# Kernel tuning notes

Measured on AMD Instinct MI355X. Metric: run time of the kernel, lower is better.

## Reference

```python
import jax, jax.numpy as jnp
import numpy as np

D_MODEL = 256
N_LEVELS = 4
N_HEADS = 8
N_POINTS = 4
HEAD_DIM = D_MODEL // N_HEADS
SPATIAL_SHAPES = np.array([[128, 128], [64, 64], [32, 32], [16, 16]], dtype=np.int64)
LEN_IN = int((SPATIAL_SHAPES[:, 0] * SPATIAL_SHAPES[:, 1]).sum())  # 21760
BATCH = 2
LEN_Q = LEN_IN  # encoder self-attention


def setup_inputs() -> dict:
    key = jax.random.key(0)
    ks = jax.random.split(key, 12)
    C = D_MODEL
    lvl_start = np.concatenate([[0], np.cumsum(SPATIAL_SHAPES[:, 0] * SPATIAL_SHAPES[:, 1])[:-1]]).astype(np.int64)
    return {
        'query': jax.random.normal(ks[0], (BATCH, LEN_Q, C), jnp.float32),
        'reference_points': jax.random.uniform(ks[1], (BATCH, LEN_Q, N_LEVELS, 2), jnp.float32),
        'input_flatten': jax.random.normal(ks[2], (BATCH, LEN_IN, C), jnp.float32),
        'input_spatial_shapes': SPATIAL_SHAPES,          # static numpy: shapes must be concrete
        'input_level_start_index': lvl_start,            # static numpy
        'Wv': jax.random.normal(ks[3], (C, C), jnp.float32) / np.sqrt(C),
        'bv': jnp.zeros((C,), jnp.float32),
        'Woff': jax.random.normal(ks[4], (C, N_HEADS * N_LEVELS * N_POINTS * 2), jnp.float32) * 0.01,
        'boff': jax.random.normal(ks[5], (N_HEADS * N_LEVELS * N_POINTS * 2,), jnp.float32) * 0.5,
        'Wa': jax.random.normal(ks[6], (C, N_HEADS * N_LEVELS * N_POINTS), jnp.float32) * 0.01,
        'ba': jnp.zeros((N_HEADS * N_LEVELS * N_POINTS,), jnp.float32),
        'Wo': jax.random.normal(ks[7], (C, C), jnp.float32) / np.sqrt(C),
        'bo': jnp.zeros((C,), jnp.float32),
    }


def _grid_sample_bilinear(v, grid):
    """v: (B,H,W,D); grid: (B,Q,P,2) in [-1,1] (x,y). align_corners=False, zero padding."""
    B, H, W, D = v.shape
    x = (grid[..., 0] + 1.0) * 0.5 * W - 0.5
    y = (grid[..., 1] + 1.0) * 0.5 * H - 0.5
    x0 = jnp.floor(x)
    y0 = jnp.floor(y)
    wx = x - x0
    wy = y - y0
    b = jnp.arange(B)[:, None, None]

    def corner(xi, yi, w):
        valid = (xi >= 0) & (xi < W) & (yi >= 0) & (yi < H)
        xi_ = jnp.clip(xi, 0, W - 1).astype(jnp.int32)
        yi_ = jnp.clip(yi, 0, H - 1).astype(jnp.int32)
        return v[b, yi_, xi_] * (w * valid)[..., None]  # (B,Q,P,D)

    return (corner(x0, y0, (1 - wx) * (1 - wy))
            + corner(x0 + 1, y0, wx * (1 - wy))
            + corner(x0, y0 + 1, (1 - wx) * wy)
            + corner(x0 + 1, y0 + 1, wx * wy))


def _msdeform_attn(query, reference_points, input_flatten, spatial_shapes_np,
                   Wv, bv, Woff, boff, Wa, ba, Wo, bo):
    N, Lq, C = query.shape
    Lin = input_flatten.shape[1]
    M, L, P, D = N_HEADS, N_LEVELS, N_POINTS, HEAD_DIM

    value = (input_flatten @ Wv + bv).reshape(N, Lin, M, D)
    offsets = (query @ Woff + boff).reshape(N, Lq, M, L, P, 2)
    attn = jax.nn.softmax((query @ Wa + ba).reshape(N, Lq, M, L * P), axis=-1).reshape(N, Lq, M, L, P)

    # sampling locations in [0,1] -> grid in [-1,1]
    grids = 2.0 * (reference_points[:, :, None, :, None, :] + offsets) - 1.0  # (N,Lq,M,L,P,2)

    out = jnp.zeros((N * M, Lq, D), value.dtype)
    start = 0
    for lid in range(L):
        H_, W_ = int(spatial_shapes_np[lid, 0]), int(spatial_shapes_np[lid, 1])
        v_l = value[:, start:start + H_ * W_]                       # (N,HW,M,D)
        v_l = v_l.transpose(0, 2, 1, 3).reshape(N * M, H_, W_, D)   # (N*M,H,W,D)
        g_l = grids[:, :, :, lid].transpose(0, 2, 1, 3, 4).reshape(N * M, Lq, P, 2)
        sampled = _grid_sample_bilinear(v_l, g_l)                   # (N*M,Lq,P,D)
        a_l = attn[:, :, :, lid].transpose(0, 2, 1, 3).reshape(N * M, Lq, P)
        out = out + jnp.einsum('bqpd,bqp->bqd', sampled, a_l)
        start += H_ * W_

    out = out.reshape(N, M, Lq, D).transpose(0, 2, 1, 3).reshape(N, Lq, M * D)
    return out @ Wo + bo


def reference(query, reference_points, input_flatten, input_spatial_shapes,
              input_level_start_index, Wv, bv, Woff, boff, Wa, ba, Wo, bo):
    spatial_np = np.asarray(input_spatial_shapes)
    return _msdeform_attn(query, reference_points, input_flatten, spatial_np,
                          Wv, bv, Woff, boff, Wa, ba, Wo, bo)
```

## Files before the change

### kernel.cpp

```cpp
#include <hip/hip_runtime.h>
#include <cstdint>
#include <cstddef>

#define LEN_IN  21760
#define BATCH   2
#define MROWS   (BATCH * LEN_IN)

typedef _Float16 hv8 __attribute__((ext_vector_type(8)));
typedef float    fv4 __attribute__((ext_vector_type(4)));

#define WAIT_LGKM0() __builtin_amdgcn_s_waitcnt(0xC07F)
#define RAW_BARRIER() __builtin_amdgcn_s_barrier()

__global__ __launch_bounds__(256) void cvt_weights(
    const float* __restrict__ Wv, const float* __restrict__ Woff,
    const float* __restrict__ Wa, const float* __restrict__ Wo,
    _Float16* __restrict__ WvT, _Float16* __restrict__ WoffT2,
    _Float16* __restrict__ WaT, _Float16* __restrict__ WoT)
{
  __shared__ float t[64][65];
  const int id = blockIdx.x, tid = threadIdx.x;
  const int c = tid & 63, r4 = tid >> 6;

  const float* src; _Float16* dst; int N; bool split = false; int nt, kt;
  if (id < 16)      { src = Wv;   dst = WvT;    N = 256; nt = id & 3;        kt = id >> 2; }
  else if (id < 32) { src = Woff; dst = WoffT2; N = 256; nt = (id - 16) & 3; kt = (id - 16) >> 2; split = true; }
  else if (id < 40) { src = Wa;   dst = WaT;    N = 128; nt = (id - 32) & 1; kt = (id - 32) >> 1; }
  else              { src = Wo;   dst = WoT;    N = 256; nt = (id - 40) & 3; kt = (id - 40) >> 2; }
  const int nb = nt * 64, kb = kt * 64;

#pragma unroll
  for (int rr = 0; rr < 16; ++rr) {
    const int r = rr * 4 + r4;
    t[r][c] = src[(size_t)(kb + r) * N + nb + c];
  }
  __syncthreads();
#pragma unroll
  for (int rr = 0; rr < 16; ++rr) {
    const int r = rr * 4 + r4;
    const float v = t[c][r];
    const _Float16 h = (_Float16)v;
    dst[(size_t)(nb + r) * 256 + kb + c] = h;
    if (split)
      dst[(size_t)(256 + nb + r) * 256 + kb + c] = (_Float16)(v - (float)h);
  }
}

template<int NTOT, int AF32, int OUTMODE>
__global__ __launch_bounds__(256) void gemm_pipe(
    const void* __restrict__ Ap, const _Float16* __restrict__ Bt,
    const float* __restrict__ bias, void* __restrict__ Cout)
{
  __shared__ _Float16 As[2][64 * 40];
  __shared__ _Float16 Bs[2][128 * 40];

  const int tid = threadIdx.x, lane = tid & 63, wave = tid >> 6;
  const int l15 = lane & 15, quad = lane >> 4;
  const int wc = wave * 32;
  const int rowBase = blockIdx.x * 64;
  const int colBase = blockIdx.y * 128;
  const int rs = tid >> 2, ks = (tid & 3) * 8;

  const float*    A32 = (const float*)Ap;
  const _Float16* A16 = (const _Float16*)Ap;

  float4 pa[3][2]; hv8 pa16[3]; hv8 pb[2][2];

  auto issueA = [&](int it) {
    const int k0 = it * 32, s = it % 3;
    if constexpr (AF32) {
      pa[s][0] = *(const float4*)&A32[(size_t)(rowBase + rs) * 256 + k0 + ks];
      pa[s][1] = *(const float4*)&A32[(size_t)(rowBase + rs) * 256 + k0 + ks + 4];
    } else {
      pa16[s] = *(const hv8*)&A16[(size_t)(rowBase + rs) * 256 + k0 + ks];
    }
  };
  auto issueB = [&](int it) {
    const int k0 = it * 32, s = it & 1;
#pragma unroll
    for (int p = 0; p < 2; ++p)
      pb[s][p] = *(const hv8*)&Bt[(size_t)(colBase + p * 64 + rs) * 256 + k0 + ks];
  };

  issueA(0); issueB(0); issueA(1); issueB(1); issueA(2);

  fv4 acc[4][2] = {};

#pragma unroll
  for (int it = 0; it < 8; ++it) {
    const int sb = it & 1, sa = it % 3;
    if constexpr (AF32) {
      const float4 f0 = pa[sa][0], f1 = pa[sa][1];
      const float fa[8] = {f0.x, f0.y, f0.z, f0.w, f1.x, f1.y, f1.z, f1.w};
      hv8 h;
#pragma unroll
      for (int e = 0; e < 8; ++e) h[e] = (_Float16)fa[e];
      *(hv8*)&As[sb][rs * 40 + ks] = h;
    } else {
      *(hv8*)&As[sb][rs * 40 + ks] = pa16[sa];
    }
#pragma unroll
    for (int p = 0; p < 2; ++p)
      *(hv8*)&Bs[sb][(p * 64 + rs) * 40 + ks] = pb[sb][p];
    if (it + 2 < 8) issueB(it + 2);
    if (it + 3 < 8) issueA(it + 3);
    WAIT_LGKM0();
    RAW_BARRIER();

    hv8 af[4];
#pragma unroll
    for (int i = 0; i < 4; ++i)
      af[i] = *(const hv8*)&As[sb][(i * 16 + l15) * 40 + quad * 8];
#pragma unroll
    for (int j = 0; j < 2; ++j) {
      const hv8 bf = *(const hv8*)&Bs[sb][(wc + j * 16 + l15) * 40 + quad * 8];
#pragma unroll
      for (int i = 0; i < 4; ++i)
        acc[i][j] = __builtin_amdgcn_mfma_f32_16x16x32_f16(af[i], bf, acc[i][j], 0, 0, 0);
    }
  }

#pragma unroll
  for (int j = 0; j < 2; ++j) {
    const int col = colBase + wc + j * 16 + l15;
    const float bj = bias[col];
#pragma unroll
    for (int i = 0; i < 4; ++i)
#pragma unroll
      for (int rg = 0; rg < 4; ++rg) {
        const int row = rowBase + i * 16 + quad * 4 + rg;
        const float v = acc[i][j][rg] + bj;
        if constexpr (OUTMODE == 0) {
          ((float*)Cout)[(size_t)row * NTOT + col] = v;
        } else if constexpr (OUTMODE == 1) {
          ((_Float16*)Cout)[(size_t)row * NTOT + col] = (_Float16)v;
        } else {
          const int n = (row >= LEN_IN) ? 1 : 0;
          const int pix = row - n * LEN_IN;
          const int m = col >> 5, d = col & 31;
          ((_Float16*)Cout)[((size_t)(n * 8 + m) * LEN_IN + pix) * 32 + d] = (_Float16)v;
        }
      }
  }
}

__global__ __launch_bounds__(256) void gemm_offs_pipe(
    const float* __restrict__ A, const _Float16* __restrict__ B2,
    const float* __restrict__ boff, const float* __restrict__ refpts,
    float* __restrict__ C)
{
  __shared__ _Float16 Ash[64 * 40], Asl[64 * 40];
  __shared__ _Float16 Bs[256 * 40];

  const int tid = threadIdx.x, lane = tid & 63, wave = tid >> 6;
  const int l15 = lane & 15, quad = lane >> 4;
  const int wc = wave * 32;
  const int rowBase = blockIdx.x * 64;
  const int colBase = blockIdx.y * 128;
  const int rs = tid >> 2, ks = (tid & 3) * 8;

  float4 pa[3][2]; hv8 pb[2][4];

  auto issueA = [&](int it) {
    const int k0 = it * 32, s = it % 3;
    pa[s][0] = *(const float4*)&A[(size_t)(rowBase + rs) * 256 + k0 + ks];
    pa[s][1] = *(const float4*)&A[(size_t)(rowBase + rs) * 256 + k0 + ks + 4];
  };
  auto issueB = [&](int it) {
    const int k0 = it * 32, s = it & 1;
#pragma unroll
    for (int p = 0; p < 4; ++p) {
      const int grow = (p < 2) ? (colBase + p * 64 + rs)
                               : (256 + colBase + (p - 2) * 64 + rs);
      pb[s][p] = *(const hv8*)&B2[(size_t)grow * 256 + k0 + ks];
    }
  };

  issueA(0); issueB(0); issueA(1); issueB(1); issueA(2);

  fv4 acc[4][2] = {};

#pragma unroll
  for (int it = 0; it < 8; ++it) {
    const int sa = it % 3, s2 = it & 1;
    {
      const float4 f0 = pa[sa][0], f1 = pa[sa][1];
      const float fa[8] = {f0.x, f0.y, f0.z, f0.w, f1.x, f1.y, f1.z, f1.w};
      hv8 hh, ll;
#pragma unroll
      for (int e = 0; e < 8; ++e) {
        hh[e] = (_Float16)fa[e];
        ll[e] = (_Float16)(fa[e] - (float)hh[e]);
      }
      *(hv8*)&Ash[rs * 40 + ks] = hh;
      *(hv8*)&Asl[rs * 40 + ks] = ll;
    }
#pragma unroll
    for (int p = 0; p < 4; ++p)
      *(hv8*)&Bs[(p * 64 + rs) * 40 + ks] = pb[s2][p];
    if (it + 2 < 8) issueB(it + 2);
    if (it + 3 < 8) issueA(it + 3);
    WAIT_LGKM0();
    RAW_BARRIER();

    hv8 ah[4], al[4];
#pragma unroll
    for (int i = 0; i < 4; ++i) {
      ah[i] = *(const hv8*)&Ash[(i * 16 + l15) * 40 + quad * 8];
      al[i] = *(const hv8*)&Asl[(i * 16 + l15) * 40 + quad * 8];
    }
#pragma unroll
    for (int j = 0; j < 2; ++j) {
      const hv8 bh = *(const hv8*)&Bs[(wc + j * 16 + l15) * 40 + quad * 8];
      const hv8 bl = *(const hv8*)&Bs[(128 + wc + j * 16 + l15) * 40 + quad * 8];
#pragma unroll
      for (int i = 0; i < 4; ++i) {
        acc[i][j] = __builtin_amdgcn_mfma_f32_16x16x32_f16(ah[i], bh, acc[i][j], 0, 0, 0);
        acc[i][j] = __builtin_amdgcn_mfma_f32_16x16x32_f16(ah[i], bl, acc[i][j], 0, 0, 0);
        acc[i][j] = __builtin_amdgcn_mfma_f32_16x16x32_f16(al[i], bh, acc[i][j], 0, 0, 0);
      }
    }
    WAIT_LGKM0();
    RAW_BARRIER();
  }

#pragma unroll
  for (int j = 0; j < 2; ++j) {
    const int c = colBase + wc + j * 16 + l15;
    const int xy = c & 1, l = (c >> 3) & 3;
    const float Wl = (float)(128 >> l);
    const float bj = boff[c];
#pragma unroll
    for (int i = 0; i < 4; ++i)
#pragma unroll
      for (int rg = 0; rg < 4; ++rg) {
        const int row = rowBase + i * 16 + quad * 4 + rg;
        const float ref = refpts[(size_t)row * 8 + l * 2 + xy];
        C[(size_t)row * 256 + c] = (acc[i][j][rg] + bj + ref) * Wl - 0.5f;
      }
  }
}

__global__ __launch_bounds__(256, 6) void sample_kernel(
    const _Float16* __restrict__ value16,
    const float* __restrict__ coords,
    const _Float16* __restrict__ logits16,
    _Float16* __restrict__ outp16)
{
  __shared__ unsigned s_pair[4096];
  __shared__ float    s_attn[1024];

  const int tid = threadIdx.x;
  const int qBase = blockIdx.x * 8;

  if (tid < 64) {
    const hv8* lp = (const hv8*)&logits16[(size_t)(qBase + (tid >> 3)) * 128 + (tid & 7) * 16];
    const hv8 w0 = lp[0], w1 = lp[1];
    float w[16];
#pragma unroll
    for (int e = 0; e < 8; ++e) { w[e] = (float)w0[e]; w[8 + e] = (float)w1[e]; }
    float mx = w[0];
#pragma unroll
    for (int i = 1; i < 16; ++i) mx = fmaxf(mx, w[i]);
    float sum = 0.f;
#pragma unroll
    for (int i = 0; i < 16; ++i) { w[i] = expf(w[i] - mx); sum += w[i]; }
    const float inv = 1.f / sum;
#pragma unroll
    for (int p = 0; p < 16; ++p) s_attn[p * 64 + tid] = w[p] * inv;
  }
  __syncthreads();

#pragma unroll
  for (int k = 0; k < 4; ++k) {
    const int i = tid + 256 * k;
    const int p = i >> 6, q = (i >> 3) & 7, m = i & 7;
    const int l = p >> 2, pp = p & 3;
    const int qg = qBase + q;
    const float2 of = *(const float2*)&coords[(size_t)qg * 256 + ((m * 4 + l) * 4 + pp) * 2];
    const float aw = s_attn[i];
    const int W = 128 >> l;
    const int st = (l == 0) ? 0 : (l == 1) ? 16384 : (l == 2) ? 20480 : 21504;
    const float xf = floorf(of.x), yf = floorf(of.y);
    const int x0 = (int)xf, y0 = (int)yf;
    const float wx = of.x - xf, wy = of.y - yf;
    uint4 rec;
    unsigned* rp = &rec.x;
#pragma unroll
    for (int c = 0; c < 4; ++c) {
      const int dx = c & 1, dy = c >> 1;
      const int xi = x0 + dx, yi = y0 + dy;
      const bool valid = (xi >= 0) & (xi < W) & (yi >= 0) & (yi < W);
      const float w = (dx ? wx : 1.f - wx) * (dy ? wy : 1.f - wy) * aw;
      union { _Float16 h; unsigned short s; } pk;
      pk.h = (_Float16)w;
      const unsigned idx = (unsigned)(st + yi * W + xi);
      rp[c] = valid ? (idx | ((unsigned)pk.s << 16)) : 0u;
    }
    *(uint4*)&s_pair[i * 4] = rec;
  }
  __syncthreads();

  const int wave = tid >> 6, lane = tid & 63;
  const int qloc = wave * 2 + (lane >> 5);
  const int sub = lane & 31, m = sub >> 2, j = sub & 3;
  const int qg = qBase + qloc;
  const int n = (qg >= LEN_IN) ? 1 : 0;
  const char* base = (const char*)value16 + (size_t)(n * 8 + m) * LEN_IN * 64 + j * 16;
  const int lb = qloc * 8 + m;

  float acc8[8] = {0.f, 0.f, 0.f, 0.f, 0.f, 0.f, 0.f, 0.f};
#pragma unroll 4
  for (int p = 0; p < 16; ++p) {
    const uint4 u4 = *(const uint4*)&s_pair[(p * 64 + lb) * 4];
    const unsigned uu[4] = {u4.x, u4.y, u4.z, u4.w};
#pragma unroll
    for (int c = 0; c < 4; ++c) {
      const unsigned u = uu[c];
      union { unsigned short s; _Float16 h; } pk;
      pk.s = (unsigned short)(u >> 16);
      const float w = (float)pk.h;
      const hv8 v = *(const hv8*)(base + (size_t)(u & 32767u) * 64);
#pragma unroll
      for (int e = 0; e < 8; ++e) acc8[e] = fmaf(w, (float)v[e], acc8[e]);
    }
  }

  hv8 o;
#pragma unroll
  for (int e = 0; e < 8; ++e) o[e] = (_Float16)acc8[e];
  *(hv8*)&outp16[(size_t)qg * 256 + m * 32 + j * 8] = o;
}

extern "C" void kernel_launch(void* const* d_in, const int* in_sizes, int n_in,
                              void* d_out, int out_size, void* d_ws, size_t ws_size,
                              hipStream_t stream) {
  const float* query   = (const float*)d_in[0];
  const float* refpts  = (const float*)d_in[1];
  const float* flatten = (const float*)d_in[2];
  const float* Wv   = (const float*)d_in[5];
  const float* bv   = (const float*)d_in[6];
  const float* Woff = (const float*)d_in[7];
  const float* boff = (const float*)d_in[8];
  const float* Wa   = (const float*)d_in[9];
  const float* ba   = (const float*)d_in[10];
  const float* Wo   = (const float*)d_in[11];
  const float* bo   = (const float*)d_in[12];
  float* out = (float*)d_out;

  const size_t NE = (size_t)MROWS * 256;
  _Float16* value16  = (_Float16*)d_ws;
  float*    coords   = (float*)(value16 + NE);
  _Float16* logits16 = (_Float16*)(coords + NE);
  _Float16* outp16   = logits16 + NE / 2;
  _Float16* WvT      = outp16 + NE;
  _Float16* WoffT2   = WvT + 256 * 256;
  _Float16* WaT      = WoffT2 + 512 * 256;
  _Float16* WoT      = WaT + 128 * 256;

  const dim3 blk(256);
  const int mtiles = MROWS / 64;

  cvt_weights<<<dim3(56), blk, 0, stream>>>(Wv, Woff, Wa, Wo, WvT, WoffT2, WaT, WoT);

  gemm_pipe<256, 1, 2><<<dim3(mtiles, 2), blk, 0, stream>>>(flatten, WvT, bv, value16);
  gemm_offs_pipe<<<dim3(mtiles, 2), blk, 0, stream>>>(query, WoffT2, boff, refpts, coords);
  gemm_pipe<128, 1, 1><<<dim3(mtiles, 1), blk, 0, stream>>>(query, WaT, ba, logits16);
  sample_kernel<<<dim3(MROWS / 8), blk, 0, stream>>>(value16, coords, logits16, outp16);
  gemm_pipe<256, 0, 0><<<dim3(mtiles, 2), blk, 0, stream>>>(outp16, WoT, bo, out);
}
```

Before: 283.8 us.

## Pre-convert activations to fp16 and fuse input GEMMs using direct global-to-LDS loads

```diff
diff --git a/kernel.cpp b/kernel.cpp
--- a/kernel.cpp
+++ b/kernel.cpp
@@ -9,8 +9,16 @@
 typedef _Float16 hv8 __attribute__((ext_vector_type(8)));
 typedef float    fv4 __attribute__((ext_vector_type(4)));
 
+#define AS1 __attribute__((address_space(1)))
+#define AS3 __attribute__((address_space(3)))
+
+#define WAIT_VM(N)   __builtin_amdgcn_s_waitcnt(0x0F70 | (N))
 #define WAIT_LGKM0() __builtin_amdgcn_s_waitcnt(0xC07F)
-#define RAW_BARRIER() __builtin_amdgcn_s_barrier()
+#define BAR()        __builtin_amdgcn_s_barrier()
+
+__device__ __forceinline__ void gl_lds16(const _Float16* g, _Float16* l) {
+  __builtin_amdgcn_global_load_lds((const AS1 void*)g, (AS3 void*)l, 16, 0, 0);
+}
 
 __global__ __launch_bounds__(256) void cvt_weights(
     const float* __restrict__ Wv, const float* __restrict__ Woff,
@@ -46,187 +54,148 @@
   }
 }
 
-template<int NTOT, int AF32, int OUTMODE>
-__global__ __launch_bounds__(256) void gemm_pipe(
-    const void* __restrict__ Ap, const _Float16* __restrict__ Bt,
-    const float* __restrict__ bias, void* __restrict__ Cout)
+__global__ __launch_bounds__(256) void cvt_acts(
+    const float* __restrict__ q, const float* __restrict__ f,
+    _Float16* __restrict__ qH, _Float16* __restrict__ qL, _Float16* __restrict__ fH)
 {
-  __shared__ _Float16 As[2][64 * 40];
-  __shared__ _Float16 Bs[2][128 * 40];
+  const size_t NE8 = (size_t)MROWS * 32;
+  const size_t id = (size_t)blockIdx.x * 256 + threadIdx.x;
+  if (id < NE8) {
+    const float4 f0 = *(const float4*)&q[id * 8];
+    const float4 f1 = *(const float4*)&q[id * 8 + 4];
+    const float fa[8] = {f0.x, f0.y, f0.z, f0.w, f1.x, f1.y, f1.z, f1.w};
+    hv8 hh, ll;
+#pragma unroll
+    for (int e = 0; e < 8; ++e) {
+      hh[e] = (_Float16)fa[e];
+      ll[e] = (_Float16)(fa[e] - (float)hh[e]);
+    }
+    *(hv8*)&qH[id * 8] = hh;
+    *(hv8*)&qL[id * 8] = ll;
+  } else {
+    const size_t e8 = id - NE8;
+    const float4 f0 = *(const float4*)&f[e8 * 8];
+    const float4 f1 = *(const float4*)&f[e8 * 8 + 4];
+    const float fa[8] = {f0.x, f0.y, f0.z, f0.w, f1.x, f1.y, f1.z, f1.w};
+    hv8 hh;
+#pragma unroll
+    for (int e = 0; e < 8; ++e) hh[e] = (_Float16)fa[e];
+    *(hv8*)&fH[e8 * 8] = hh;
+  }
+}
+
+__global__ __launch_bounds__(256) void gemm3(
+    const _Float16* __restrict__ fH, const _Float16* __restrict__ qH,
+    const _Float16* __restrict__ qL,
+    const _Float16* __restrict__ WvT, const _Float16* __restrict__ WoffT2,
+    const _Float16* __restrict__ WaT,
+    const float* __restrict__ bv, const float* __restrict__ boff,
+    const float* __restrict__ ba, const float* __restrict__ refpts,
+    _Float16* __restrict__ value16, float* __restrict__ coords,
+    _Float16* __restrict__ logits16)
+{
+  __shared__ _Float16 L[2][8192];
 
   const int tid = threadIdx.x, lane = tid & 63, wave = tid >> 6;
   const int l15 = lane & 15, quad = lane >> 4;
-  const int wc = wave * 32;
+  const int r4 = lane >> 2, k4 = (lane & 3) * 8;
   const int rowBase = blockIdx.x * 64;
-  const int colBase = blockIdx.y * 128;
-  const int rs = tid >> 2, ks = (tid & 3) * 8;
-
-  const float*    A32 = (const float*)Ap;
-  const _Float16* A16 = (const _Float16*)Ap;
-
-  float4 pa[3][2]; hv8 pa16[3]; hv8 pb[2][2];
-
-  auto issueA = [&](int it) {
-    const int k0 = it * 32, s = it % 3;
-    if constexpr (AF32) {
-      pa[s][0] = *(const float4*)&A32[(size_t)(rowBase + rs) * 256 + k0 + ks];
-      pa[s][1] = *(const float4*)&A32[(size_t)(rowBase + rs) * 256 + k0 + ks + 4];
-    } else {
-      pa16[s] = *(const hv8*)&A16[(size_t)(rowBase + rs) * 256 + k0 + ks];
-    }
-  };
-  auto issueB = [&](int it) {
-    const int k0 = it * 32, s = it & 1;
-#pragma unroll
-    for (int p = 0; p < 2; ++p)
-      pb[s][p] = *(const hv8*)&Bt[(size_t)(colBase + p * 64 + rs) * 256 + k0 + ks];
-  };
-
-  issueA(0); issueB(0); issueA(1); issueB(1); issueA(2);
-
-  fv4 acc[4][2] = {};
-
-#pragma unroll
-  for (int it = 0; it < 8; ++it) {
-    const int sb = it & 1, sa = it % 3;
-    if constexpr (AF32) {
-      const float4 f0 = pa[sa][0], f1 = pa[sa][1];
-      const float fa[8] = {f0.x, f0.y, f0.z, f0.w, f1.x, f1.y, f1.z, f1.w};
-      hv8 h;
-#pragma unroll
-      for (int e = 0; e < 8; ++e) h[e] = (_Float16)fa[e];
-      *(hv8*)&As[sb][rs * 40 + ks] = h;
-    } else {
-      *(hv8*)&As[sb][rs * 40 + ks] = pa16[sa];
-    }
-#pragma unroll
-    for (int p = 0; p < 2; ++p)
-      *(hv8*)&Bs[sb][(p * 64 + rs) * 40 + ks] = pb[sb][p];
-    if (it + 2 < 8) issueB(it + 2);
-    if (it + 3 < 8) issueA(it + 3);
-    WAIT_LGKM0();
-    RAW_BARRIER();
-
-    hv8 af[4];
-#pragma unroll
-    for (int i = 0; i < 4; ++i)
-      af[i] = *(const hv8*)&As[sb][(i * 16 + l15) * 40 + quad * 8];
+  const int y = blockIdx.y;
+
+  if (y < 2 || y == 6) {
+    const _Float16* A  = (y == 6) ? qH : fH;
+    const _Float16* Bt = (y == 6) ? WaT : WvT;
+    const int colBase  = (y == 6) ? 0 : y * 128;
+
+    auto issue = [&](int it) {
+      const int buf = it & 1, k0 = it * 32;
+      gl_lds16(&A [(size_t)(rowBase + wave * 16 + r4) * 256 + k0 + k4], &L[buf][(wave * 16) * 32]);
+      gl_lds16(&Bt[(size_t)(colBase + wave * 32 + r4) * 256 + k0 + k4], &L[buf][2048 + (wave * 32) * 32]);
+      gl_lds16(&Bt[(size_t)(colBase + wave * 32 + 16 + r4) * 256 + k0 + k4], &L[buf][2048 + (wave * 32 + 16) * 32]);
+    };
+    issue(0); issue(1);
+
+    fv4 acc[4][2] = {};
+#pragma unroll
+    for (int it = 0; it < 8; ++it) {
+      const int buf = it & 1;
+      if (it == 7) WAIT_VM(0); else WAIT_VM(3);
+      BAR();
+      hv8 af[4];
+#pragma unroll
+      for (int i = 0; i < 4; ++i)
+        af[i] = *(const hv8*)&L[buf][(i * 16 + l15) * 32 + quad * 8];
+#pragma unroll
+      for (int j = 0; j < 2; ++j) {
+        const hv8 bf = *(const hv8*)&L[buf][2048 + (wave * 32 + j * 16 + l15) * 32 + quad * 8];
+#pragma unroll
+        for (int i = 0; i < 4; ++i)
+          acc[i][j] = __builtin_amdgcn_mfma_f32_16x16x32_f16(af[i], bf, acc[i][j], 0, 0, 0);
+      }
+      WAIT_LGKM0();
+      BAR();
+      if (it + 2 < 8) issue(it + 2);
+    }
+
+    const float* bias = (y == 6) ? ba : bv;
 #pragma unroll
     for (int j = 0; j < 2; ++j) {
-      const hv8 bf = *(const hv8*)&Bs[sb][(wc + j * 16 + l15) * 40 + quad * 8];
+      const int col = colBase + wave * 32 + j * 16 + l15;
+      const float bj = bias[col];
 #pragma unroll
       for (int i = 0; i < 4; ++i)
-        acc[i][j] = __builtin_amdgcn_mfma_f32_16x16x32_f16(af[i], bf, acc[i][j], 0, 0, 0);
-    }
-  }
-
-#pragma unroll
-  for (int j = 0; j < 2; ++j) {
-    const int col = colBase + wc + j * 16 + l15;
-    const float bj = bias[col];
-#pragma unroll
-    for (int i = 0; i < 4; ++i)
-#pragma unroll
-      for (int rg = 0; rg < 4; ++rg) {
-        const int row = rowBase + i * 16 + quad * 4 + rg;
-        const float v = acc[i][j][rg] + bj;
-        if constexpr (OUTMODE == 0) {
-          ((float*)Cout)[(size_t)row * NTOT + col] = v;
-        } else if constexpr (OUTMODE == 1) {
-          ((_Float16*)Cout)[(size_t)row * NTOT + col] = (_Float16)v;
-        } else {
-          const int n = (row >= LEN_IN) ? 1 : 0;
-          const int pix = row - n * LEN_IN;
-          const int m = col >> 5, d = col & 31;
-          ((_Float16*)Cout)[((size_t)(n * 8 + m) * LEN_IN + pix) * 32 + d] = (_Float16)v;
+#pragma unroll
+        for (int rg = 0; rg < 4; ++rg) {
+          const int row = rowBase + i * 16 + quad * 4 + rg;
+          const float v = acc[i][j][rg] + bj;
+          if (y == 6) {
+            logits16[(size_t)row * 128 + col] = (_Float16)v;
+          } else {
+            const int n = (row >= LEN_IN) ? 1 : 0;
+            const int pix = row - n * LEN_IN;
+            const int m = col >> 5, d = col & 31;
+            value16[((size_t)(n * 8 + m) * LEN_IN + pix) * 32 + d] = (_Float16)v;
+          }
         }
+    }
+  } else {
+    const int c0 = (y - 2) * 64;
+
+    auto issue = [&](int it) {
+      const int buf = it & 1, k0 = it * 32;
+      gl_lds16(&qH[(size_t)(rowBase + wave * 16 + r4) * 256 + k0 + k4], &L[buf][(wave * 16) * 32]);
+      gl_lds16(&qL[(size_t)(rowBase + wave * 16 + r4) * 256 + k0 + k4], &L[buf][2048 + (wave * 16) * 32]);
+      gl_lds16(&WoffT2[(size_t)(c0 + wave * 16 + r4) * 256 + k0 + k4], &L[buf][4096 + (wave * 16) * 32]);
+      gl_lds16(&WoffT2[(size_t)(256 + c0 + wave * 16 + r4) * 256 + k0 + k4], &L[buf][4096 + (64 + wave * 16) * 32]);
+    };
+    issue(0); issue(1);
+
+    fv4 acc[4] = {};
+#pragma unroll
+    for (int it = 0; it < 8; ++it) {
+      const int buf = it & 1;
+      if (it == 7) WAIT_VM(0); else WAIT_VM(4);
+      BAR();
+      hv8 ah[4], al[4];
+#pragma unroll
+      for (int i = 0; i < 4; ++i) {
+        ah[i] = *(const hv8*)&L[buf][(i * 16 + l15) * 32 + quad * 8];
+        al[i] = *(const hv8*)&L[buf][2048 + (i * 16 + l15) * 32 + quad * 8];
       }
-  }
-}
-
-__global__ __launch_bounds__(256) void gemm_offs_pipe(
-    const float* __restrict__ A, const _Float16* __restrict__ B2,
-    const float* __restrict__ boff, const float* __restrict__ refpts,
-    float* __restrict__ C)
-{
-  __shared__ _Float16 Ash[64 * 40], Asl[64 * 40];
-  __shared__ _Float16 Bs[256 * 40];
-
-  const int tid = threadIdx.x, lane = tid & 63, wave = tid >> 6;
-  const int l15 = lane & 15, quad = lane >> 4;
-  const int wc = wave * 32;
-  const int rowBase = blockIdx.x * 64;
-  const int colBase = blockIdx.y * 128;
-  const int rs = tid >> 2, ks = (tid & 3) * 8;
-
-  float4 pa[3][2]; hv8 pb[2][4];
-
-  auto issueA = [&](int it) {
-    const int k0 = it * 32, s = it % 3;
-    pa[s][0] = *(const float4*)&A[(size_t)(rowBase + rs) * 256 + k0 + ks];
-    pa[s][1] = *(const float4*)&A[(size_t)(rowBase + rs) * 256 + k0 + ks + 4];
-  };
-  auto issueB = [&](int it) {
-    const int k0 = it * 32, s = it & 1;
-#pragma unroll
-    for (int p = 0; p < 4; ++p) {
-      const int grow = (p < 2) ? (colBase + p * 64 + rs)
-                               : (256 + colBase + (p - 2) * 64 + rs);
-      pb[s][p] = *(const hv8*)&B2[(size_t)grow * 256 + k0 + ks];
-    }
-  };
-
-  issueA(0); issueB(0); issueA(1); issueB(1); issueA(2);
-
-  fv4 acc[4][2] = {};
-
-#pragma unroll
-  for (int it = 0; it < 8; ++it) {
-    const int sa = it % 3, s2 = it & 1;
-    {
-      const float4 f0 = pa[sa][0], f1 = pa[sa][1];
-      const float fa[8] = {f0.x, f0.y, f0.z, f0.w, f1.x, f1.y, f1.z, f1.w};
-      hv8 hh, ll;
-#pragma unroll
-      for (int e = 0; e < 8; ++e) {
-        hh[e] = (_Float16)fa[e];
-        ll[e] = (_Float16)(fa[e] - (float)hh[e]);
+      const hv8 bh = *(const hv8*)&L[buf][4096 + (wave * 16 + l15) * 32 + quad * 8];
+      const hv8 bl = *(const hv8*)&L[buf][4096 + (64 + wave * 16 + l15) * 32 + quad * 8];
+#pragma unroll
+      for (int i = 0; i < 4; ++i) {
+        acc[i] = __builtin_amdgcn_mfma_f32_16x16x32_f16(ah[i], bh, acc[i], 0, 0, 0);
+        acc[i] = __builtin_amdgcn_mfma_f32_16x16x32_f16(ah[i], bl, acc[i], 0, 0, 0);
+        acc[i] = __builtin_amdgcn_mfma_f32_16x16x32_f16(al[i], bh, acc[i], 0, 0, 0);
       }
-      *(hv8*)&Ash[rs * 40 + ks] = hh;
-      *(hv8*)&Asl[rs * 40 + ks] = ll;
-    }
-#pragma unroll
-    for (int p = 0; p < 4; ++p)
-      *(hv8*)&Bs[(p * 64 + rs) * 40 + ks] = pb[s2][p];
-    if (it + 2 < 8) issueB(it + 2);
-    if (it + 3 < 8) issueA(it + 3);
-    WAIT_LGKM0();
-    RAW_BARRIER();
-
-    hv8 ah[4], al[4];
-#pragma unroll
-    for (int i = 0; i < 4; ++i) {
-      ah[i] = *(const hv8*)&Ash[(i * 16 + l15) * 40 + quad * 8];
-      al[i] = *(const hv8*)&Asl[(i * 16 + l15) * 40 + quad * 8];
-    }
-#pragma unroll
-    for (int j = 0; j < 2; ++j) {
-      const hv8 bh = *(const hv8*)&Bs[(wc + j * 16 + l15) * 40 + quad * 8];
-      const hv8 bl = *(const hv8*)&Bs[(128 + wc + j * 16 + l15) * 40 + quad * 8];
-#pragma unroll
-      for (int i = 0; i < 4; ++i) {
-        acc[i][j] = __builtin_amdgcn_mfma_f32_16x16x32_f16(ah[i], bh, acc[i][j], 0, 0, 0);
-        acc[i][j] = __builtin_amdgcn_mfma_f32_16x16x32_f16(ah[i], bl, acc[i][j], 0, 0, 0);
-        acc[i][j] = __builtin_amdgcn_mfma_f32_16x16x32_f16(al[i], bh, acc[i][j], 0, 0, 0);
-      }
-    }
-    WAIT_LGKM0();
-    RAW_BARRIER();
-  }
-
-#pragma unroll
-  for (int j = 0; j < 2; ++j) {
-    const int c = colBase + wc + j * 16 + l15;
+      WAIT_LGKM0();
+      BAR();
+      if (it + 2 < 8) issue(it + 2);
+    }
+
+    const int c = c0 + wave * 16 + l15;
     const int xy = c & 1, l = (c >> 3) & 3;
     const float Wl = (float)(128 >> l);
     const float bj = boff[c];
@@ -236,7 +205,63 @@
       for (int rg = 0; rg < 4; ++rg) {
         const int row = rowBase + i * 16 + quad * 4 + rg;
         const float ref = refpts[(size_t)row * 8 + l * 2 + xy];
-        C[(size_t)row * 256 + c] = (acc[i][j][rg] + bj + ref) * Wl - 0.5f;
+        coords[(size_t)row * 256 + c] = (acc[i][rg] + bj + ref) * Wl - 0.5f;
+      }
+  }
+}
+
+__global__ __launch_bounds__(256) void gemm_out(
+    const _Float16* __restrict__ A, const _Float16* __restrict__ Bt,
+    const float* __restrict__ bias, float* __restrict__ C)
+{
+  __shared__ _Float16 L[2][6144];
+
+  const int tid = threadIdx.x, lane = tid & 63, wave = tid >> 6;
+  const int l15 = lane & 15, quad = lane >> 4;
+  const int r4 = lane >> 2, k4 = (lane & 3) * 8;
+  const int rowBase = blockIdx.x * 64;
+  const int colBase = blockIdx.y * 128;
+
+  auto issue = [&](int it) {
+    const int buf = it & 1, k0 = it * 32;
+    gl_lds16(&A [(size_t)(rowBase + wave * 16 + r4) * 256 + k0 + k4], &L[buf][(wave * 16) * 32]);
+    gl_lds16(&Bt[(size_t)(colBase + wave * 32 + r4) * 256 + k0 + k4], &L[buf][2048 + (wave * 32) * 32]);
+    gl_lds16(&Bt[(size_t)(colBase + wave * 32 + 16 + r4) * 256 + k0 + k4], &L[buf][2048 + (wave * 32 + 16) * 32]);
+  };
+  issue(0); issue(1);
+
+  fv4 acc[4][2] = {};
+#pragma unroll
+  for (int it = 0; it < 8; ++it) {
+    const int buf = it & 1;
+    if (it == 7) WAIT_VM(0); else WAIT_VM(3);
+    BAR();
+    hv8 af[4];
+#pragma unroll
+    for (int i = 0; i < 4; ++i)
+      af[i] = *(const hv8*)&L[buf][(i * 16 + l15) * 32 + quad * 8];
+#pragma unroll
+    for (int j = 0; j < 2; ++j) {
+      const hv8 bf = *(const hv8*)&L[buf][2048 + (wave * 32 + j * 16 + l15) * 32 + quad * 8];
+#pragma unroll
+      for (int i = 0; i < 4; ++i)
+        acc[i][j] = __builtin_amdgcn_mfma_f32_16x16x32_f16(af[i], bf, acc[i][j], 0, 0, 0);
+    }
+    WAIT_LGKM0();
+    BAR();
+    if (it + 2 < 8) issue(it + 2);
+  }
+
+#pragma unroll
+  for (int j = 0; j < 2; ++j) {
+    const int col = colBase + wave * 32 + j * 16 + l15;
+    const float bj = bias[col];
+#pragma unroll
+    for (int i = 0; i < 4; ++i)
+#pragma unroll
+      for (int rg = 0; rg < 4; ++rg) {
+        const int row = rowBase + i * 16 + quad * 4 + rg;
+        C[(size_t)row * 256 + col] = acc[i][j][rg] + bj;
       }
   }
 }
@@ -352,20 +377,24 @@
   _Float16* value16  = (_Float16*)d_ws;
   float*    coords   = (float*)(value16 + NE);
   _Float16* logits16 = (_Float16*)(coords + NE);
-  _Float16* outp16   = logits16 + NE / 2;
-  _Float16* WvT      = outp16 + NE;
+  _Float16* qH       = logits16 + NE / 2;
+  _Float16* qL       = qH + NE;
+  _Float16* fH       = qL + NE;
+  _Float16* outp16   = fH;
+  _Float16* WvT      = fH + NE;
   _Float16* WoffT2   = WvT + 256 * 256;
   _Float16* WaT      = WoffT2 + 512 * 256;
   _Float16* WoT      = WaT + 128 * 256;
 
   const dim3 blk(256);
-  const int mtiles = MROWS / 64;
 
   cvt_weights<<<dim3(56), blk, 0, stream>>>(Wv, Woff, Wa, Wo, WvT, WoffT2, WaT, WoT);
-
-  gemm_pipe<256, 1, 2><<<dim3(mtiles, 2), blk, 0, stream>>>(flatten, WvT, bv, value16);
-  gemm_offs_pipe<<<dim3(mtiles, 2), blk, 0, stream>>>(query, WoffT2, boff, refpts, coords);
-  gemm_pipe<128, 1, 1><<<dim3(mtiles, 1), blk, 0, stream>>>(query, WaT, ba, logits16);
+  cvt_acts<<<dim3(10880), blk, 0, stream>>>(query, flatten, qH, qL, fH);
+
+  gemm3<<<dim3(MROWS / 64, 7), blk, 0, stream>>>(fH, qH, qL, WvT, WoffT2, WaT,
+      bv, boff, ba, refpts, value16, coords, logits16);
+
   sample_kernel<<<dim3(MROWS / 8), blk, 0, stream>>>(value16, coords, logits16, outp16);
-  gemm_pipe<256, 0, 0><<<dim3(mtiles, 2), blk, 0, stream>>>(outp16, WoT, bo, out);
-}
+
+  gemm_out<<<dim3(MROWS / 64, 2), blk, 0, stream>>>(outp16, WoT, bo, out);
+}
```

Result: slower. 292.0 us (+2.9%).
